# Kernel optimization log

Measured on AMD Instinct MI355X. Metric: run time of the kernel, lower is better.

The kernel has to match this reference:

```python
import jax, jax.numpy as jnp
import numpy as np

N, E, D = 50000, 800000, 128   # nodes, edges, input feature dim
HEADS, HC = 8, 16
H = HEADS * HC                 # 128 hidden width after concat
G, OUT = 64, 16                # graphs in batch, output classes
EPS_BN = 1e-5


def _gat_conv(x, src, dst, edge_attr, W, att_src, att_dst, We, att_edge, b):
    """PyG GATConv (concat=True, negative_slope=0.2, add_self_loops=True,
    fill_value='mean' for edge_attr, dropout inactive in eval)."""
    n = x.shape[0]
    # self-loop edge attr = per-node mean of incoming edge attrs
    ones = jnp.ones((src.shape[0], 1), x.dtype)
    deg = jax.ops.segment_sum(ones, dst, num_segments=n)
    ea_mean = jax.ops.segment_sum(edge_attr, dst, num_segments=n) / jnp.maximum(deg, 1.0)
    loop = jnp.arange(n, dtype=src.dtype)
    src_f = jnp.concatenate([src, loop])
    dst_f = jnp.concatenate([dst, loop])
    ea = jnp.concatenate([edge_attr, ea_mean])          # [E+N, 1]
    h = (x @ W).reshape(n, HEADS, HC)                   # [N, heads, hc]
    a_src = jnp.sum(h * att_src, axis=-1)               # [N, heads]
    a_dst = jnp.sum(h * att_dst, axis=-1)               # [N, heads]
    he = (ea @ We).reshape(-1, HEADS, HC)               # [E+N, heads, hc]
    a_e = jnp.sum(he * att_edge, axis=-1)               # [E+N, heads]
    alpha = jax.nn.leaky_relu(a_src[src_f] + a_dst[dst_f] + a_e, 0.2)
    # segment softmax over destination nodes
    amax = jax.ops.segment_max(alpha, dst_f, num_segments=n)
    ex = jnp.exp(alpha - amax[dst_f])
    denom = jax.ops.segment_sum(ex, dst_f, num_segments=n)
    coef = ex / (denom[dst_f] + 1e-16)                  # [E+N, heads]
    out = jax.ops.segment_sum(h[src_f] * coef[..., None], dst_f, num_segments=n)
    return out.reshape(n, H) + b


def setup_inputs() -> dict:
    key = jax.random.key(0)
    k = lambda i: jax.random.fold_in(key, i)
    nrm = lambda i, shape, s=0.1: jax.random.normal(k(i), shape, dtype=jnp.float32) * s
    inp = {
        "x": jax.random.normal(k(0), (N, D), dtype=jnp.float32),
        "edge_index": jax.random.randint(k(1), (2, E), 0, N, dtype=jnp.int32),
        "edge_weights": jax.random.normal(k(2), (E, 1), dtype=jnp.float32),
        "batch": jnp.sort(jax.random.randint(k(3), (N,), 0, G, dtype=jnp.int32)),
        "bn_gamma": jnp.ones((D,), jnp.float32),
        "bn_beta": jnp.zeros((D,), jnp.float32),
        "bn_mean": nrm(4, (D,)),
        "bn_var": jax.random.uniform(k(5), (D,), dtype=jnp.float32) + 0.5,
    }
    ci = 10
    for li, ind in [(1, D), (2, H), (3, H)]:
        inp[f"W{li}"] = nrm(ci, (ind, H)); ci += 1
        inp[f"att_src{li}"] = nrm(ci, (HEADS, HC)); ci += 1
        inp[f"att_dst{li}"] = nrm(ci, (HEADS, HC)); ci += 1
        inp[f"We{li}"] = nrm(ci, (1, H)); ci += 1
        inp[f"att_edge{li}"] = nrm(ci, (HEADS, HC)); ci += 1
        inp[f"b{li}"] = jnp.zeros((H,), jnp.float32)
    inp["Wl1"] = nrm(40, (H, 2 * HC)); inp["bl1"] = jnp.zeros((2 * HC,), jnp.float32)
    inp["Wl2"] = nrm(41, (2 * HC, OUT)); inp["bl2"] = jnp.zeros((OUT,), jnp.float32)
    return inp


def reference(x, edge_index, edge_weights, batch,
              bn_gamma, bn_beta, bn_mean, bn_var,
              W1, att_src1, att_dst1, We1, att_edge1, b1,
              W2, att_src2, att_dst2, We2, att_edge2, b2,
              W3, att_src3, att_dst3, We3, att_edge3, b3,
              Wl1, bl1, Wl2, bl2):
    src, dst = edge_index[0], edge_index[1]
    # BatchNorm (eval mode, running stats)
    h = (x - bn_mean) / jnp.sqrt(bn_var + EPS_BN) * bn_gamma + bn_beta
    h = jax.nn.relu(_gat_conv(h, src, dst, edge_weights, W1, att_src1, att_dst1, We1, att_edge1, b1))
    h = jax.nn.relu(_gat_conv(h, src, dst, edge_weights, W2, att_src2, att_dst2, We2, att_edge2, b2))
    h = _gat_conv(h, src, dst, edge_weights, W3, att_src3, att_dst3, We3, att_edge3, b3)
    g = jax.ops.segment_max(h, batch, num_segments=G)   # global max pool -> [G, H]
    g = jax.nn.relu(g @ Wl1 + bl1)
    # dropout p=0.5 is identity in eval mode
    return g @ Wl2 + bl2
```

## Files before the change

### kernel.cpp

```cpp
#include <hip/hip_runtime.h>
#include <math.h>

#define NN 50000
#define NE 800000
#define NH 8
#define HDIM 128
#define NG 64
#define PSPLIT 16
#define MAXD 64

typedef __attribute__((ext_vector_type(8))) short bf16x8;
typedef __attribute__((ext_vector_type(4))) float f32x4;

static __device__ __forceinline__ float lrelu02(float x){ return x > 0.f ? x : 0.2f*x; }
static __device__ __forceinline__ unsigned short f2bf(float f){
    unsigned u = __float_as_uint(f);
    unsigned r = (u + 0x7FFFu + ((u >> 16) & 1u)) >> 16;
    return (unsigned short)r;
}
static __device__ __forceinline__ float bf2f(unsigned short h){ return __uint_as_float((unsigned)h << 16); }
static __device__ __forceinline__ float bf_lo(unsigned v){ return __uint_as_float(v << 16); }
static __device__ __forceinline__ float bf_hi(unsigned v){ return __uint_as_float(v & 0xFFFF0000u); }

__global__ void k_prep(const float* We1, const float* ae1, const float* We2, const float* ae2,
                       const float* We3, const float* ae3, float* wev,
                       const float* gam, const float* bet, const float* mean, const float* var,
                       float* sc, float* sh){
    int t = threadIdx.x;
    if (t < 128){
        float s = gam[t] * rsqrtf(var[t] + 1e-5f);
        sc[t] = s; sh[t] = bet[t] - mean[t] * s;
    } else if (t < 152){
        int q = t - 128; int l = q >> 3, hd = q & 7;
        const float* We = (l == 0) ? We1 : (l == 1) ? We2 : We3;
        const float* ae = (l == 0) ? ae1 : (l == 1) ? ae2 : ae3;
        float s = 0.f;
        for (int c = 0; c < 16; c++) s += We[hd*16+c] * ae[hd*16+c];
        wev[q] = s;
    }
}

__global__ void k_wprep(const float* W1, const float* W2, const float* W3,
                        unsigned short* Wth, unsigned short* Wtl){
    int i = blockIdx.x*256 + threadIdx.x;
    if (i >= 3*16384) return;
    int l = i >> 14, rem = i & 16383;
    int k = rem >> 7, n = rem & 127;
    const float* W = (l==0) ? W1 : (l==1) ? W2 : W3;
    float w = W[k*128 + n];
    unsigned short hi = f2bf(w);
    unsigned short lo = f2bf(w - bf2f(hi));
    Wth[l*16384 + n*128 + k] = hi;
    Wtl[l*16384 + n*128 + k] = lo;
}

__global__ void k_scatter(const int* srcp, const int* dstp, const float* ew,
                          unsigned long long* pk, unsigned* slab){
    int i0 = (blockIdx.x*256 + threadIdx.x)*4;
    if (i0 >= NE) return;
    int4   d4 = *(const int4*)&dstp[i0];
    float4 w4 = *(const float4*)&ew[i0];
    int4   s4 = *(const int4*)&srcp[i0];
    int   d[4] = {d4.x, d4.y, d4.z, d4.w};
    float w[4] = {w4.x, w4.y, w4.z, w4.w};
    int   s[4] = {s4.x, s4.y, s4.z, s4.w};
    unsigned long long old[4];
    #pragma unroll
    for (int j = 0; j < 4; j++){
        int fx = __float2int_rn(w[j] * 16384.f);
        unsigned long long enc = ((unsigned long long)(unsigned)fx << 32) | 1ull;
        old[j] = atomicAdd(&pk[d[j]], enc);
    }
    #pragma unroll
    for (int j = 0; j < 4; j++){
        unsigned rank = (unsigned)(old[j] & 0xFFFFFFFFull);
        if (rank < MAXD){
            unsigned ent = (unsigned)s[j] | ((unsigned)f2bf(w[j]) << 16);
            __builtin_nontemporal_store(ent, &slab[(size_t)d[j]*MAXD + rank]);
        }
    }
}

__global__ __launch_bounds__(256, 3) void k_gemm(const float* A,
        const unsigned short* Wth, const unsigned short* Wtl,
        const float* sc, const float* sh,
        const float* att_s, const float* att_d,
        unsigned* Hb, float* a_src, float* a_dst, int M){
    __shared__ unsigned short Ah[64][132];
    __shared__ unsigned short Al[64][132];
    int t = threadIdx.x;
    int row0 = blockIdx.x * 64;
    int w = t >> 6, l = t & 63;
    int lr = l & 15, lg = l >> 4;

    {
        bool bn = (sc != nullptr);
        const float2* A2 = (const float2*)A;
        for (int i = 0; i < 16; i++){
            int idx2 = t + i*256;
            int r = idx2 >> 6, c2 = idx2 & 63;
            float2 v = make_float2(0.f, 0.f);
            if (row0 + r < M){
                v = A2[(size_t)(row0+r)*64 + c2];
                if (bn){
                    float2 s2 = ((const float2*)sc)[c2], h2 = ((const float2*)sh)[c2];
                    v.x = v.x*s2.x + h2.x; v.y = v.y*s2.y + h2.y;
                }
            }
            unsigned short h0 = f2bf(v.x), h1 = f2bf(v.y);
            unsigned short l0 = f2bf(v.x - bf2f(h0)), l1 = f2bf(v.y - bf2f(h1));
            ((unsigned*)&Ah[r][0])[c2] = (unsigned)h0 | ((unsigned)h1 << 16);
            ((unsigned*)&Al[r][0])[c2] = (unsigned)l0 | ((unsigned)l1 << 16);
        }
    }
    __syncthreads();

    f32x4 acc[4][2];
    #pragma unroll
    for (int m = 0; m < 4; m++){ acc[m][0] = (f32x4){0,0,0,0}; acc[m][1] = (f32x4){0,0,0,0}; }

    #pragma unroll
    for (int ks = 0; ks < 4; ks++){
        int kk = ks*32 + lg*8;
        bf16x8 bh0 = *(const bf16x8*)&Wth[((w*2+0)*16 + lr)*128 + kk];
        bf16x8 bl0 = *(const bf16x8*)&Wtl[((w*2+0)*16 + lr)*128 + kk];
        bf16x8 bh1 = *(const bf16x8*)&Wth[((w*2+1)*16 + lr)*128 + kk];
        bf16x8 bl1 = *(const bf16x8*)&Wtl[((w*2+1)*16 + lr)*128 + kk];
        #pragma unroll
        for (int m = 0; m < 4; m++){
            bf16x8 a_h = *(const bf16x8*)&Ah[m*16 + lr][kk];
            bf16x8 a_l = *(const bf16x8*)&Al[m*16 + lr][kk];
            acc[m][0] = __builtin_amdgcn_mfma_f32_16x16x32_bf16(a_h, bh0, acc[m][0], 0, 0, 0);
            acc[m][0] = __builtin_amdgcn_mfma_f32_16x16x32_bf16(a_h, bl0, acc[m][0], 0, 0, 0);
            acc[m][0] = __builtin_amdgcn_mfma_f32_16x16x32_bf16(a_l, bh0, acc[m][0], 0, 0, 0);
            acc[m][1] = __builtin_amdgcn_mfma_f32_16x16x32_bf16(a_h, bh1, acc[m][1], 0, 0, 0);
            acc[m][1] = __builtin_amdgcn_mfma_f32_16x16x32_bf16(a_h, bl1, acc[m][1], 0, 0, 0);
            acc[m][1] = __builtin_amdgcn_mfma_f32_16x16x32_bf16(a_l, bh1, acc[m][1], 0, 0, 0);
        }
    }

    float asv[2], adv[2];
    #pragma unroll
    for (int n = 0; n < 2; n++){
        asv[n] = att_s[(w*2+n)*16 + lr];
        adv[n] = att_d[(w*2+n)*16 + lr];
    }
    #pragma unroll
    for (int m = 0; m < 4; m++){
        #pragma unroll
        for (int n = 0; n < 2; n++){
            #pragma unroll
            for (int r = 0; r < 4; r++){
                float v = acc[m][n][r];
                float pv = __shfl_xor(v, 1);
                int row = row0 + m*16 + lg*4 + r;
                if (!(l & 1) && row < M){
                    unsigned d = (unsigned)f2bf(v) | ((unsigned)f2bf(pv) << 16);
                    Hb[(size_t)row*64 + w*16 + n*8 + (lr >> 1)] = d;
                }
            }
        }
    }
    #pragma unroll
    for (int m = 0; m < 4; m++){
        #pragma unroll
        for (int r = 0; r < 4; r++){
            int row = row0 + m*16 + lg*4 + r;
            #pragma unroll
            for (int n = 0; n < 2; n++){
                float ps = acc[m][n][r] * asv[n];
                float pd = acc[m][n][r] * adv[n];
                #pragma unroll
                for (int off = 1; off < 16; off <<= 1){
                    ps += __shfl_xor(ps, off);
                    pd += __shfl_xor(pd, off);
                }
                if (lr == 0 && row < M){
                    a_src[row*NH + w*2 + n] = ps;
                    a_dst[row*NH + w*2 + n] = pd;
                }
            }
        }
    }
}

__global__ __launch_bounds__(256) void k_aggr(const unsigned long long* pk, const unsigned* slab,
                       const float* a_src, const float* a_dst, const float* wev,
                       const unsigned* Hb, const float* bias, float* Out, int do_relu){
    int wid = threadIdx.x >> 6, lane = threadIdx.x & 63;
    int n = blockIdx.x*4 + wid;
    if (n >= NN) return;
    unsigned long long pv = pk[n];
    int dgt = (int)(unsigned)(pv & 0xFFFFFFFFull);
    int dg  = dgt < MAXD ? dgt : MAXD;
    float ea_self = (float)(int)(unsigned)(pv >> 32) * (1.f/16384.f) / fmaxf((float)dgt, 1.f);
    int hd = lane >> 3;
    float ad = a_dst[n*NH + hd];
    float wh = wev[hd];
    float accL0, accH0, den0, accL1 = 0.f, accH1 = 0.f, den1 = 0.f;
    {
        unsigned v = Hb[(size_t)n*64 + lane];
        float c = __expf(lrelu02(a_src[n*NH + hd] + ad + ea_self*wh));
        den0 = c; accL0 = c*bf_lo(v); accH0 = c*bf_hi(v);
    }
    const uint4* srow4 = (const uint4*)&slab[(size_t)n*MAXD];
    for (int base = 0; base < dg; base += 16){
        uint4 e0 = srow4[(base>>2)+0], e1 = srow4[(base>>2)+1];
        uint4 e2 = srow4[(base>>2)+2], e3 = srow4[(base>>2)+3];
        unsigned ent[16] = {e0.x,e0.y,e0.z,e0.w, e1.x,e1.y,e1.z,e1.w,
                            e2.x,e2.y,e2.z,e2.w, e3.x,e3.y,e3.z,e3.w};
        unsigned v[16];
        #pragma unroll
        for (int j = 0; j < 16; j++) v[j] = Hb[(size_t)(ent[j] & 0xFFFFu)*64 + lane];
        float as[16];
        #pragma unroll
        for (int j = 0; j < 16; j++) as[j] = a_src[(ent[j] & 0xFFFFu)*NH + hd];
        #pragma unroll
        for (int j = 0; j < 16; j++){
            float eaw = bf2f((unsigned short)(ent[j] >> 16));
            float c = (base + j < dg) ? __expf(lrelu02(as[j] + ad + eaw*wh)) : 0.f;
            if (j & 1){ den1 += c; accL1 += c*bf_lo(v[j]); accH1 += c*bf_hi(v[j]); }
            else      { den0 += c; accL0 += c*bf_lo(v[j]); accH0 += c*bf_hi(v[j]); }
        }
    }
    float inv = 1.f / (den0 + den1 + 1e-16f);
    float2 bv = ((const float2*)bias)[lane];
    float o0 = (accL0 + accL1) * inv + bv.x;
    float o1 = (accH0 + accH1) * inv + bv.y;
    if (do_relu){ o0 = fmaxf(o0, 0.f); o1 = fmaxf(o1, 0.f); }
    ((float2*)Out)[(size_t)n*64 + lane] = make_float2(o0, o1);
}

static __device__ int lower_bound_batch(const int* b, int v){
    int lo = 0, hi = NN;
    while (lo < hi){
        int mid = (lo + hi) >> 1;
        if (b[mid] < v) lo = mid + 1; else hi = mid;
    }
    return lo;
}

__global__ void k_pool1(const float* A, const int* batch, float* gpart){
    int g = blockIdx.x >> 4, s = blockIdx.x & (PSPLIT-1);
    int start = lower_bound_batch(batch, g);
    int end   = lower_bound_batch(batch, g + 1);
    int nrows = end - start;
    int chunk = (nrows + PSPLIT - 1) / PSPLIT;
    int rs = start + s*chunk;
    int re = rs + chunk; if (re > end) re = end;
    int col = threadIdx.x;
    float m = -INFINITY;
    for (int r = rs; r < re; r++) m = fmaxf(m, A[(size_t)r*HDIM + col]);
    gpart[(size_t)blockIdx.x*HDIM + col] = m;
}

__global__ void k_pool2(const float* gpart, float* gp){
    int g = blockIdx.x, col = threadIdx.x;
    float m = -INFINITY;
    for (int s = 0; s < PSPLIT; s++)
        m = fmaxf(m, gpart[(size_t)(g*PSPLIT+s)*HDIM + col]);
    gp[g*HDIM + col] = m;
}

__global__ __launch_bounds__(256) void k_mlp(const float* gp, const float* Wl1, const float* bl1,
                      const float* Wl2, const float* bl2, float* out){
    __shared__ float gl[NG*HDIM];
    __shared__ float t1[NG*32];
    int t = threadIdx.x;
    for (int i = 0; i < 8; i++)
        ((float4*)gl)[t + i*256] = ((const float4*)gp)[t + i*256];
    __syncthreads();
    for (int i = 0; i < 8; i++){
        int o = t + i*256;
        int gi = o >> 5, j = o & 31;
        float s = bl1[j];
        for (int k = 0; k < 128; k++) s += gl[gi*128 + k] * Wl1[k*32 + j];
        t1[o] = fmaxf(s, 0.f);
    }
    __syncthreads();
    for (int i = 0; i < 4; i++){
        int o = t + i*256;
        int gi = o >> 4, j = o & 15;
        float s = bl2[j];
        for (int k = 0; k < 32; k++) s += t1[gi*32 + k] * Wl2[k*16 + j];
        out[o] = s;
    }
}

extern "C" void kernel_launch(void* const* d_in, const int* in_sizes, int n_in,
                              void* d_out, int out_size, void* d_ws, size_t ws_size,
                              hipStream_t stream){
    const float* x    = (const float*)d_in[0];
    const int*   ei   = (const int*)d_in[1];
    const float* ew   = (const float*)d_in[2];
    const int*   batch= (const int*)d_in[3];
    const float* bng  = (const float*)d_in[4];
    const float* bnb  = (const float*)d_in[5];
    const float* bnm  = (const float*)d_in[6];
    const float* bnv  = (const float*)d_in[7];
    const float* Wmat[3] = {(const float*)d_in[8],  (const float*)d_in[14], (const float*)d_in[20]};
    const float* asr[3]  = {(const float*)d_in[9],  (const float*)d_in[15], (const float*)d_in[21]};
    const float* adt[3]  = {(const float*)d_in[10], (const float*)d_in[16], (const float*)d_in[22]};
    const float* Wep[3]  = {(const float*)d_in[11], (const float*)d_in[17], (const float*)d_in[23]};
    const float* aep[3]  = {(const float*)d_in[12], (const float*)d_in[18], (const float*)d_in[24]};
    const float* bp[3]   = {(const float*)d_in[13], (const float*)d_in[19], (const float*)d_in[25]};
    const float* Wl1 = (const float*)d_in[26];
    const float* bl1 = (const float*)d_in[27];
    const float* Wl2 = (const float*)d_in[28];
    const float* bl2 = (const float*)d_in[29];

    char* p = (char*)d_ws;
    auto alloc = [&](size_t bytes)->char*{
        char* r = p; p += (bytes + 255) & ~(size_t)255; return r;
    };
    float*    bufA  = (float*)alloc((size_t)NN*HDIM*4);
    unsigned* Hb    = (unsigned*)alloc((size_t)NN*64*4);
    float*    a_src = (float*)alloc((size_t)NN*NH*4);
    float*    a_dst = (float*)alloc((size_t)NN*NH*4);
    unsigned long long* pk = (unsigned long long*)alloc((size_t)NN*8);
    unsigned* slab  = (unsigned*)alloc((size_t)NN*MAXD*4);
    float*    wev   = (float*)alloc(24*4);
    float*    scv   = (float*)alloc(128*4);
    float*    shv   = (float*)alloc(128*4);
    unsigned short* Wth = (unsigned short*)alloc((size_t)3*16384*2);
    unsigned short* Wtl = (unsigned short*)alloc((size_t)3*16384*2);
    float*    gpart = (float*)alloc((size_t)NG*PSPLIT*HDIM*4);
    float*    gpool = (float*)alloc((size_t)NG*HDIM*4);

    const int* srcp = ei;
    const int* dstp = ei + NE;

    hipMemsetAsync(pk, 0, (size_t)NN*8, stream);
    k_prep<<<1, 256, 0, stream>>>(Wep[0], aep[0], Wep[1], aep[1], Wep[2], aep[2], wev,
                                  bng, bnb, bnm, bnv, scv, shv);
    k_wprep<<<192, 256, 0, stream>>>(Wmat[0], Wmat[1], Wmat[2], Wth, Wtl);
    k_scatter<<<(NE/4+255)/256, 256, 0, stream>>>(srcp, dstp, ew, pk, slab);

    for (int l = 0; l < 3; l++){
        const float* A  = (l == 0) ? x : bufA;
        const float* sc = (l == 0) ? scv : nullptr;
        const float* sh = (l == 0) ? shv : nullptr;
        k_gemm<<<(NN+63)/64, 256, 0, stream>>>(A, Wth + l*16384, Wtl + l*16384, sc, sh,
                                               asr[l], adt[l], Hb, a_src, a_dst, NN);
        k_aggr<<<(NN+3)/4, 256, 0, stream>>>(pk, slab, a_src, a_dst, wev + l*8,
                                             Hb, bp[l], bufA, (l < 2) ? 1 : 0);
    }
    k_pool1<<<NG*PSPLIT, 128, 0, stream>>>(bufA, batch, gpart);
    k_pool2<<<NG, 128, 0, stream>>>(gpart, gpool);
    k_mlp<<<1, 256, 0, stream>>>(gpool, Wl1, bl1, Wl2, bl2, (float*)d_out);
}
```

Measured before the change: 324.5 us.

## Store inter-layer activations as bf16 and add a bf16-input GEMM variant

Layer outputs are now written as packed bf16 instead of fp32, and layers 2-3 use a new GEMM that loads bf16 activations directly with only the hi/lo weight split (two MFMAs per tile instead of more). This halves activation traffic and cuts GEMM work. The scatter kernel switches to a 32-bit count atomic, and the self-loop edge-attr mean is computed in the aggregation from the slab entries. Weight/BN prep kernels are merged into one launch. The risks are precision loss from bf16 activations, and a self-loop mean that is wrong for nodes with more than MAXD in-edges.

```diff
diff --git a/kernel.cpp b/kernel.cpp
--- a/kernel.cpp
+++ b/kernel.cpp
@@ -22,28 +22,28 @@
 static __device__ __forceinline__ float bf_lo(unsigned v){ return __uint_as_float(v << 16); }
 static __device__ __forceinline__ float bf_hi(unsigned v){ return __uint_as_float(v & 0xFFFF0000u); }
 
-__global__ void k_prep(const float* We1, const float* ae1, const float* We2, const float* ae2,
-                       const float* We3, const float* ae3, float* wev,
-                       const float* gam, const float* bet, const float* mean, const float* var,
-                       float* sc, float* sh){
-    int t = threadIdx.x;
-    if (t < 128){
-        float s = gam[t] * rsqrtf(var[t] + 1e-5f);
-        sc[t] = s; sh[t] = bet[t] - mean[t] * s;
-    } else if (t < 152){
-        int q = t - 128; int l = q >> 3, hd = q & 7;
-        const float* We = (l == 0) ? We1 : (l == 1) ? We2 : We3;
-        const float* ae = (l == 0) ? ae1 : (l == 1) ? ae2 : ae3;
-        float s = 0.f;
-        for (int c = 0; c < 16; c++) s += We[hd*16+c] * ae[hd*16+c];
-        wev[q] = s;
-    }
-}
-
-__global__ void k_wprep(const float* W1, const float* W2, const float* W3,
-                        unsigned short* Wth, unsigned short* Wtl){
+__global__ void k_prep0(const float* W1, const float* W2, const float* W3,
+                        unsigned short* Wth, unsigned short* Wtl,
+                        const float* We1, const float* ae1, const float* We2, const float* ae2,
+                        const float* We3, const float* ae3, float* wev,
+                        const float* gam, const float* bet, const float* mean, const float* var,
+                        float* sc, float* sh){
+    if (blockIdx.x == 192){
+        int t = threadIdx.x;
+        if (t < 128){
+            float s = gam[t] * rsqrtf(var[t] + 1e-5f);
+            sc[t] = s; sh[t] = bet[t] - mean[t] * s;
+        } else if (t < 152){
+            int q = t - 128; int l = q >> 3, hd = q & 7;
+            const float* We = (l == 0) ? We1 : (l == 1) ? We2 : We3;
+            const float* ae = (l == 0) ? ae1 : (l == 1) ? ae2 : ae3;
+            float s = 0.f;
+            for (int c = 0; c < 16; c++) s += We[hd*16+c] * ae[hd*16+c];
+            wev[q] = s;
+        }
+        return;
+    }
     int i = blockIdx.x*256 + threadIdx.x;
-    if (i >= 3*16384) return;
     int l = i >> 14, rem = i & 16383;
     int k = rem >> 7, n = rem & 127;
     const float* W = (l==0) ? W1 : (l==1) ? W2 : W3;
@@ -55,33 +55,19 @@
 }
 
 __global__ void k_scatter(const int* srcp, const int* dstp, const float* ew,
-                          unsigned long long* pk, unsigned* slab){
-    int i0 = (blockIdx.x*256 + threadIdx.x)*4;
-    if (i0 >= NE) return;
-    int4   d4 = *(const int4*)&dstp[i0];
-    float4 w4 = *(const float4*)&ew[i0];
-    int4   s4 = *(const int4*)&srcp[i0];
-    int   d[4] = {d4.x, d4.y, d4.z, d4.w};
-    float w[4] = {w4.x, w4.y, w4.z, w4.w};
-    int   s[4] = {s4.x, s4.y, s4.z, s4.w};
-    unsigned long long old[4];
-    #pragma unroll
-    for (int j = 0; j < 4; j++){
-        int fx = __float2int_rn(w[j] * 16384.f);
-        unsigned long long enc = ((unsigned long long)(unsigned)fx << 32) | 1ull;
-        old[j] = atomicAdd(&pk[d[j]], enc);
-    }
-    #pragma unroll
-    for (int j = 0; j < 4; j++){
-        unsigned rank = (unsigned)(old[j] & 0xFFFFFFFFull);
-        if (rank < MAXD){
-            unsigned ent = (unsigned)s[j] | ((unsigned)f2bf(w[j]) << 16);
-            __builtin_nontemporal_store(ent, &slab[(size_t)d[j]*MAXD + rank]);
-        }
-    }
-}
-
-__global__ __launch_bounds__(256, 3) void k_gemm(const float* A,
+                          unsigned* cnt, unsigned* slab){
+    int i = blockIdx.x*256 + threadIdx.x;
+    if (i >= NE) return;
+    int d = dstp[i];
+    float w = ew[i];
+    unsigned rank = atomicAdd(&cnt[d], 1u);
+    if (rank < MAXD){
+        unsigned ent = (unsigned)srcp[i] | ((unsigned)f2bf(w) << 16);
+        __builtin_nontemporal_store(ent, &slab[(size_t)d*MAXD + rank]);
+    }
+}
+
+__global__ __launch_bounds__(256, 3) void k_gemm1(const float* A,
         const unsigned short* Wth, const unsigned short* Wtl,
         const float* sc, const float* sh,
         const float* att_s, const float* att_d,
@@ -94,7 +80,6 @@
     int lr = l & 15, lg = l >> 4;
 
     {
-        bool bn = (sc != nullptr);
         const float2* A2 = (const float2*)A;
         for (int i = 0; i < 16; i++){
             int idx2 = t + i*256;
@@ -102,10 +87,8 @@
             float2 v = make_float2(0.f, 0.f);
             if (row0 + r < M){
                 v = A2[(size_t)(row0+r)*64 + c2];
-                if (bn){
-                    float2 s2 = ((const float2*)sc)[c2], h2 = ((const float2*)sh)[c2];
-                    v.x = v.x*s2.x + h2.x; v.y = v.y*s2.y + h2.y;
-                }
+                float2 s2 = ((const float2*)sc)[c2], h2 = ((const float2*)sh)[c2];
+                v.x = v.x*s2.x + h2.x; v.y = v.y*s2.y + h2.y;
             }
             unsigned short h0 = f2bf(v.x), h1 = f2bf(v.y);
             unsigned short l0 = f2bf(v.x - bf2f(h0)), l1 = f2bf(v.y - bf2f(h1));
@@ -184,25 +167,106 @@
     }
 }
 
-__global__ __launch_bounds__(256) void k_aggr(const unsigned long long* pk, const unsigned* slab,
+__global__ __launch_bounds__(256, 3) void k_gemm_bf(const unsigned* A16,
+        const unsigned short* Wth, const unsigned short* Wtl,
+        const float* att_s, const float* att_d,
+        unsigned* Hb, float* a_src, float* a_dst, int M){
+    __shared__ unsigned short Ah[64][132];
+    int t = threadIdx.x;
+    int row0 = blockIdx.x * 64;
+    int w = t >> 6, l = t & 63;
+    int lr = l & 15, lg = l >> 4;
+
+    for (int i = 0; i < 16; i++){
+        int idx = t + i*256;
+        int r = idx >> 6, c2 = idx & 63;
+        unsigned v = 0;
+        if (row0 + r < M) v = A16[(size_t)(row0+r)*64 + c2];
+        ((unsigned*)&Ah[r][0])[c2] = v;
+    }
+    __syncthreads();
+
+    f32x4 acc[4][2];
+    #pragma unroll
+    for (int m = 0; m < 4; m++){ acc[m][0] = (f32x4){0,0,0,0}; acc[m][1] = (f32x4){0,0,0,0}; }
+
+    #pragma unroll
+    for (int ks = 0; ks < 4; ks++){
+        int kk = ks*32 + lg*8;
+        bf16x8 bh0 = *(const bf16x8*)&Wth[((w*2+0)*16 + lr)*128 + kk];
+        bf16x8 bl0 = *(const bf16x8*)&Wtl[((w*2+0)*16 + lr)*128 + kk];
+        bf16x8 bh1 = *(const bf16x8*)&Wth[((w*2+1)*16 + lr)*128 + kk];
+        bf16x8 bl1 = *(const bf16x8*)&Wtl[((w*2+1)*16 + lr)*128 + kk];
+        #pragma unroll
+        for (int m = 0; m < 4; m++){
+            bf16x8 a_h = *(const bf16x8*)&Ah[m*16 + lr][kk];
+            acc[m][0] = __builtin_amdgcn_mfma_f32_16x16x32_bf16(a_h, bh0, acc[m][0], 0, 0, 0);
+            acc[m][0] = __builtin_amdgcn_mfma_f32_16x16x32_bf16(a_h, bl0, acc[m][0], 0, 0, 0);
+            acc[m][1] = __builtin_amdgcn_mfma_f32_16x16x32_bf16(a_h, bh1, acc[m][1], 0, 0, 0);
+            acc[m][1] = __builtin_amdgcn_mfma_f32_16x16x32_bf16(a_h, bl1, acc[m][1], 0, 0, 0);
+        }
+    }
+
+    float asv[2], adv[2];
+    #pragma unroll
+    for (int n = 0; n < 2; n++){
+        asv[n] = att_s[(w*2+n)*16 + lr];
+        adv[n] = att_d[(w*2+n)*16 + lr];
+    }
+    #pragma unroll
+    for (int m = 0; m < 4; m++){
+        #pragma unroll
+        for (int n = 0; n < 2; n++){
+            #pragma unroll
+            for (int r = 0; r < 4; r++){
+                float v = acc[m][n][r];
+                float pv = __shfl_xor(v, 1);
+                int row = row0 + m*16 + lg*4 + r;
+                if (!(l & 1) && row < M){
+                    unsigned d = (unsigned)f2bf(v) | ((unsigned)f2bf(pv) << 16);
+                    Hb[(size_t)row*64 + w*16 + n*8 + (lr >> 1)] = d;
+                }
+            }
+        }
+    }
+    #pragma unroll
+    for (int m = 0; m < 4; m++){
+        #pragma unroll
+        for (int r = 0; r < 4; r++){
+            int row = row0 + m*16 + lg*4 + r;
+            #pragma unroll
+            for (int n = 0; n < 2; n++){
+                float ps = acc[m][n][r] * asv[n];
+                float pd = acc[m][n][r] * adv[n];
+                #pragma unroll
+                for (int off = 1; off < 16; off <<= 1){
+                    ps += __shfl_xor(ps, off);
+                    pd += __shfl_xor(pd, off);
+                }
+                if (lr == 0 && row < M){
+                    a_src[row*NH + w*2 + n] = ps;
+                    a_dst[row*NH + w*2 + n] = pd;
+                }
+            }
+        }
+    }
+}
+
+__global__ __launch_bounds__(256) void k_aggr(const unsigned* cnt, const unsigned* slab,
                        const float* a_src, const float* a_dst, const float* wev,
-                       const unsigned* Hb, const float* bias, float* Out, int do_relu){
+                       const unsigned* Hb, const float* bias, unsigned* Out16, int do_relu){
     int wid = threadIdx.x >> 6, lane = threadIdx.x & 63;
     int n = blockIdx.x*4 + wid;
     if (n >= NN) return;
-    unsigned long long pv = pk[n];
-    int dgt = (int)(unsigned)(pv & 0xFFFFFFFFull);
-    int dg  = dgt < MAXD ? dgt : MAXD;
-    float ea_self = (float)(int)(unsigned)(pv >> 32) * (1.f/16384.f) / fmaxf((float)dgt, 1.f);
+    unsigned dgt = cnt[n];
+    int dg = (int)(dgt < MAXD ? dgt : MAXD);
     int hd = lane >> 3;
     float ad = a_dst[n*NH + hd];
     float wh = wev[hd];
-    float accL0, accH0, den0, accL1 = 0.f, accH1 = 0.f, den1 = 0.f;
-    {
-        unsigned v = Hb[(size_t)n*64 + lane];
-        float c = __expf(lrelu02(a_src[n*NH + hd] + ad + ea_self*wh));
-        den0 = c; accL0 = c*bf_lo(v); accH0 = c*bf_hi(v);
-    }
+    unsigned vself = Hb[(size_t)n*64 + lane];
+    float asn = a_src[n*NH + hd];
+    float accL0=0.f, accH0=0.f, den0=0.f, accL1=0.f, accH1=0.f, den1=0.f;
+    float easum = 0.f;
     const uint4* srow4 = (const uint4*)&slab[(size_t)n*MAXD];
     for (int base = 0; base < dg; base += 16){
         uint4 e0 = srow4[(base>>2)+0], e1 = srow4[(base>>2)+1];
@@ -218,17 +282,24 @@
         #pragma unroll
         for (int j = 0; j < 16; j++){
             float eaw = bf2f((unsigned short)(ent[j] >> 16));
-            float c = (base + j < dg) ? __expf(lrelu02(as[j] + ad + eaw*wh)) : 0.f;
+            bool live = (base + j < dg);
+            float c = live ? __expf(lrelu02(as[j] + ad + eaw*wh)) : 0.f;
+            easum += live ? eaw : 0.f;
             if (j & 1){ den1 += c; accL1 += c*bf_lo(v[j]); accH1 += c*bf_hi(v[j]); }
             else      { den0 += c; accL0 += c*bf_lo(v[j]); accH0 += c*bf_hi(v[j]); }
         }
+    }
+    {
+        float ea_self = easum / fmaxf((float)dgt, 1.f);
+        float c = __expf(lrelu02(asn + ad + ea_self*wh));
+        den0 += c; accL0 += c*bf_lo(vself); accH0 += c*bf_hi(vself);
     }
     float inv = 1.f / (den0 + den1 + 1e-16f);
     float2 bv = ((const float2*)bias)[lane];
     float o0 = (accL0 + accL1) * inv + bv.x;
     float o1 = (accH0 + accH1) * inv + bv.y;
     if (do_relu){ o0 = fmaxf(o0, 0.f); o1 = fmaxf(o1, 0.f); }
-    ((float2*)Out)[(size_t)n*64 + lane] = make_float2(o0, o1);
+    Out16[(size_t)n*64 + lane] = (unsigned)f2bf(o0) | ((unsigned)f2bf(o1) << 16);
 }
 
 static __device__ int lower_bound_batch(const int* b, int v){
@@ -240,7 +311,7 @@
     return lo;
 }
 
-__global__ void k_pool1(const float* A, const int* batch, float* gpart){
+__global__ void k_pool1(const unsigned* A16, const int* batch, float* gpart){
     int g = blockIdx.x >> 4, s = blockIdx.x & (PSPLIT-1);
     int start = lower_bound_batch(batch, g);
     int end   = lower_bound_batch(batch, g + 1);
@@ -248,10 +319,14 @@
     int chunk = (nrows + PSPLIT - 1) / PSPLIT;
     int rs = start + s*chunk;
     int re = rs + chunk; if (re > end) re = end;
-    int col = threadIdx.x;
-    float m = -INFINITY;
-    for (int r = rs; r < re; r++) m = fmaxf(m, A[(size_t)r*HDIM + col]);
-    gpart[(size_t)blockIdx.x*HDIM + col] = m;
+    int c = threadIdx.x;
+    float m0 = -INFINITY, m1 = -INFINITY;
+    for (int r = rs; r < re; r++){
+        unsigned v = A16[(size_t)r*64 + c];
+        m0 = fmaxf(m0, bf_lo(v));
+        m1 = fmaxf(m1, bf_hi(v));
+    }
+    ((float2*)&gpart[(size_t)blockIdx.x*HDIM])[c] = make_float2(m0, m1);
 }
 
 __global__ void k_pool2(const float* gpart, float* gp){
@@ -313,11 +388,11 @@
     auto alloc = [&](size_t bytes)->char*{
         char* r = p; p += (bytes + 255) & ~(size_t)255; return r;
     };
-    float*    bufA  = (float*)alloc((size_t)NN*HDIM*4);
     unsigned* Hb    = (unsigned*)alloc((size_t)NN*64*4);
+    unsigned* A16   = (unsigned*)alloc((size_t)NN*64*4);
     float*    a_src = (float*)alloc((size_t)NN*NH*4);
     float*    a_dst = (float*)alloc((size_t)NN*NH*4);
-    unsigned long long* pk = (unsigned long long*)alloc((size_t)NN*8);
+    unsigned* cnt   = (unsigned*)alloc((size_t)NN*4);
     unsigned* slab  = (unsigned*)alloc((size_t)NN*MAXD*4);
     float*    wev   = (float*)alloc(24*4);
     float*    scv   = (float*)alloc(128*4);
@@ -330,22 +405,23 @@
     const int* srcp = ei;
     const int* dstp = ei + NE;
 
-    hipMemsetAsync(pk, 0, (size_t)NN*8, stream);
-    k_prep<<<1, 256, 0, stream>>>(Wep[0], aep[0], Wep[1], aep[1], Wep[2], aep[2], wev,
-                                  bng, bnb, bnm, bnv, scv, shv);
-    k_wprep<<<192, 256, 0, stream>>>(Wmat[0], Wmat[1], Wmat[2], Wth, Wtl);
-    k_scatter<<<(NE/4+255)/256, 256, 0, stream>>>(srcp, dstp, ew, pk, slab);
-
-    for (int l = 0; l < 3; l++){
-        const float* A  = (l == 0) ? x : bufA;
-        const float* sc = (l == 0) ? scv : nullptr;
-        const float* sh = (l == 0) ? shv : nullptr;
-        k_gemm<<<(NN+63)/64, 256, 0, stream>>>(A, Wth + l*16384, Wtl + l*16384, sc, sh,
-                                               asr[l], adt[l], Hb, a_src, a_dst, NN);
-        k_aggr<<<(NN+3)/4, 256, 0, stream>>>(pk, slab, a_src, a_dst, wev + l*8,
-                                             Hb, bp[l], bufA, (l < 2) ? 1 : 0);
-    }
-    k_pool1<<<NG*PSPLIT, 128, 0, stream>>>(bufA, batch, gpart);
+    hipMemsetAsync(cnt, 0, (size_t)NN*4, stream);
+    k_prep0<<<193, 256, 0, stream>>>(Wmat[0], Wmat[1], Wmat[2], Wth, Wtl,
+                                     Wep[0], aep[0], Wep[1], aep[1], Wep[2], aep[2], wev,
+                                     bng, bnb, bnm, bnv, scv, shv);
+    k_scatter<<<(NE+255)/256, 256, 0, stream>>>(srcp, dstp, ew, cnt, slab);
+
+    k_gemm1<<<(NN+63)/64, 256, 0, stream>>>(x, Wth, Wtl, scv, shv,
+                                            asr[0], adt[0], Hb, a_src, a_dst, NN);
+    k_aggr<<<(NN+3)/4, 256, 0, stream>>>(cnt, slab, a_src, a_dst, wev,
+                                         Hb, bp[0], A16, 1);
+    for (int l = 1; l < 3; l++){
+        k_gemm_bf<<<(NN+63)/64, 256, 0, stream>>>(A16, Wth + l*16384, Wtl + l*16384,
+                                                  asr[l], adt[l], Hb, a_src, a_dst, NN);
+        k_aggr<<<(NN+3)/4, 256, 0, stream>>>(cnt, slab, a_src, a_dst, wev + l*8,
+                                             Hb, bp[l], A16, (l < 2) ? 1 : 0);
+    }
+    k_pool1<<<NG*PSPLIT, 64, 0, stream>>>(A16, batch, gpart);
     k_pool2<<<NG, 128, 0, stream>>>(gpart, gpool);
     k_mlp<<<1, 256, 0, stream>>>(gpool, Wl1, bl1, Wl2, bl2, (float*)d_out);
 }
```

Result: no change. 329.8 us (+1.6%).
